# Kernel optimization log

Hardware: AMD Instinct MI355X
Metric: run time of the kernel (lower is better)

## Reference

```python
import jax, jax.numpy as jnp
from jax import lax
import numpy as np

CIN, COUT, K, STYLE_DIM = 256, 256, 3, 512
N_LAYERS = 4
TYPES = ("same", "upsample", "same", "downsample")
SCALE = 1.0 / float(np.sqrt(CIN * K ** 2))  # source uses kernel_size**2 even in 1D
EPS = 1e-8
_BK = np.array([1.0, 3.0, 3.0, 1.0], dtype=np.float32)
BLUR_K = _BK / _BK.sum()  # normalized FIR kernel, len 4


def _blur(x, kern, pad):
    # x: (B, C, L); depthwise FIR correlation after zero-padding (upfirdn1d, up=down=1)
    B, C, _ = x.shape
    xp = jnp.pad(x, ((0, 0), (0, 0), (pad[0], pad[1])))
    w = jnp.broadcast_to(kern.astype(x.dtype)[None, None, :], (C, 1, kern.shape[0]))
    return lax.conv_general_dilated(xp, w, (1,), 'VALID', feature_group_count=C,
                                    dimension_numbers=('NCH', 'OIH', 'NCH'))


def _conv_same(x, w):
    # x: (Cin, L), w: (Cout, Cin, K); padding = (K-1)//2, stride 1
    p = (K - 1) // 2
    return lax.conv_general_dilated(x[None], w, (1,), [(p, p)],
                                    dimension_numbers=('NCH', 'OIH', 'NCH'))[0]


def _conv_down(x, w):
    # stride-2 valid conv (padding handled by preceding blur)
    return lax.conv_general_dilated(x[None], w, (2,), 'VALID',
                                    dimension_numbers=('NCH', 'OIH', 'NCH'))[0]


def _conv_up(x, w_t):
    # torch conv_transpose1d(stride=2, padding=0); w_t: (Cin, Cout, K)
    return lax.conv_transpose(x[None], w_t, (2,), 'VALID',
                              dimension_numbers=('NCH', 'IOH', 'NCH'),
                              transpose_kernel=True)[0]


def _layer(x, style, w, b, mw, mb, typ):
    # style modulation: s = Linear(style) -> (B, Cin)
    s = style @ mw.T + mb
    weight = (SCALE * w) * s[:, None, :, None]              # (B, Cout, Cin, K)
    demod = lax.rsqrt(jnp.sum(weight * weight, axis=(2, 3)) + EPS)
    weight = weight * demod[:, :, None, None]
    blur_k = jnp.asarray(BLUR_K)
    if typ == 'same':
        out = jax.vmap(_conv_same)(x, weight) + b[None, :, None]
    elif typ == 'upsample':
        # bias added by conv_transpose BEFORE blur (kernel_scale=2, pad=(1,1) for k=3, kb=4)
        out = jax.vmap(_conv_up)(x, weight.transpose(0, 2, 1, 3)) + b[None, :, None]
        out = _blur(out, 2.0 * blur_k, (1, 1))
    elif typ == 'downsample':
        # blur first (kernel_scale=1, pad=(2,2) for k=3, kb=4), then stride-2 conv
        xb = _blur(x, blur_k, (2, 2))
        out = jax.vmap(_conv_down)(xb, weight) + b[None, :, None]
    else:
        raise NotImplementedError(typ)
    return out


def setup_inputs() -> dict:
    key = jax.random.key(0)
    ks = jax.random.split(key, 6)
    B, L = 16, 4096
    return {
        'x': jax.random.normal(ks[0], (B, CIN, L), dtype=jnp.float32),
        'style': jax.random.normal(ks[1], (B, STYLE_DIM), dtype=jnp.float32),
        'weights': jax.random.normal(ks[2], (N_LAYERS, COUT, CIN, K), dtype=jnp.float32),
        'biases': jax.random.normal(ks[3], (N_LAYERS, COUT), dtype=jnp.float32) * 0.1,
        'mod_w': jax.random.normal(ks[4], (N_LAYERS, CIN, STYLE_DIM), dtype=jnp.float32) / np.sqrt(STYLE_DIM),
        'mod_b': 1.0 + 0.1 * jax.random.normal(ks[5], (N_LAYERS, CIN), dtype=jnp.float32),
    }


def reference(x, style, weights, biases, mod_w, mod_b):
    out = x
    for i, typ in enumerate(TYPES):
        out = _layer(out, style, weights[i], biases[i], mod_w[i], mod_b[i], typ)
    return out
```

## Files before the change

kernel.cpp:

```cpp
#include <hip/hip_runtime.h>
#include <math.h>
#include <stddef.h>

#define CIN 256
#define COUT 256
#define SD 512
#define NB 16
#define KSCALE (1.0f / 48.0f)
#define MEPS 1e-8f
#define SRROW 8320

typedef __attribute__((ext_vector_type(8))) short short8;
typedef __attribute__((ext_vector_type(4))) float floatx4;
typedef unsigned short ushort;

__device__ inline ushort f2bf(float f) {
    union { float f; unsigned int u; } v; v.f = f;
    unsigned int u = v.u;
    return (ushort)((u + 0x7FFFu + ((u >> 16) & 1u)) >> 16);
}
__device__ inline float bf2f(ushort h) {
    union { unsigned int u; float f; } v; v.u = ((unsigned int)h) << 16;
    return v.f;
}

__device__ inline void gload16(const ushort* g, ushort* l) {
    __builtin_amdgcn_global_load_lds(
        (const __attribute__((address_space(1))) unsigned int*)g,
        (__attribute__((address_space(3))) unsigned int*)l,
        16, 0, 0);
}

__global__ __launch_bounds__(256) void mod_k(
    const float* __restrict__ style, const float* __restrict__ weights,
    const float* __restrict__ mod_w, const float* __restrict__ mod_b,
    float* __restrict__ s_all, float* __restrict__ demod_all)
{
    int layer = blockIdx.x >> 4;
    int b = blockIdx.x & 15;
    int t = threadIdx.x;
    __shared__ float st[SD];
    __shared__ float s2[CIN];

    for (int j = t; j < SD; j += 256) st[j] = style[b * SD + j];
    __syncthreads();

    const float* mw = mod_w + ((size_t)layer * CIN + t) * SD;
    float acc = 0.f;
    for (int j = 0; j < SD; ++j) acc += mw[j] * st[j];
    float s = acc + mod_b[layer * CIN + t];
    s_all[((size_t)layer * NB + b) * CIN + t] = s;
    s2[t] = s * s;
    __syncthreads();

    const float* wr = weights + ((size_t)layer * COUT + t) * (CIN * 3);
    float d = 0.f;
    for (int ci = 0; ci < CIN; ++ci) {
        float w0 = wr[ci * 3 + 0], w1 = wr[ci * 3 + 1], w2 = wr[ci * 3 + 2];
        d += (w0 * w0 + w1 * w1 + w2 * w2) * s2[ci];
    }
    demod_all[((size_t)layer * NB + b) * CIN + t] = rsqrtf(KSCALE * KSCALE * d + MEPS);
}

__global__ __launch_bounds__(256) void wprep_k(
    const float* __restrict__ weights, ushort* __restrict__ Wbf)
{
    int layer = blockIdx.y;
    int idx = blockIdx.x * 256 + threadIdx.x;
    int a = idx >> 8, c = idx & 255;
    ushort* wl = Wbf + (size_t)layer * 196608;
    if (layer == 1) {
        const float* src = weights + ((size_t)1 * 196608) + ((size_t)c * 256 + a) * 3;
        #pragma unroll
        for (int k = 0; k < 3; ++k)
            wl[(size_t)k * 65536 + a * 256 + c] = f2bf(src[k]);
    } else {
        const float* src = weights + ((size_t)layer * 196608) + ((size_t)a * 256 + c) * 3;
        #pragma unroll
        for (int k = 0; k < 3; ++k)
            wl[(size_t)a * 768 + k * 256 + c] = f2bf(src[k]);
    }
}

__global__ __launch_bounds__(256) void xprep_k(
    const float* __restrict__ x, const float* __restrict__ s0,
    ushort* __restrict__ Tout)
{
    __shared__ ushort lt[64 * 72];
    int l0 = blockIdx.x * 64, ci0 = blockIdx.y * 64;
    int b = blockIdx.z;
    int t = threadIdx.x;
    const float* xb = x + (size_t)b * CIN * 4096;
    const float* sb = s0 + b * CIN;

    for (int idx = t; idx < 64 * 64; idx += 256) {
        int ci = idx >> 6, lc = idx & 63;
        float v = xb[(size_t)(ci0 + ci) * 4096 + l0 + lc] * sb[ci0 + ci];
        lt[lc * 72 + ci] = f2bf(v);
    }
    __syncthreads();
    ushort* ob = Tout + (size_t)b * SRROW * 256;
    for (int idx = t; idx < 64 * 8; idx += 256) {
        int lc = idx >> 3, ch = idx & 7;
        short8 v = *(const short8*)&lt[lc * 72 + ch * 8];
        *(short8*)&ob[(size_t)(l0 + lc) * 256 + ci0 + ch * 8] = v;
    }
}

__global__ __launch_bounds__(256) void guard_k(
    ushort* __restrict__ T, int rowA, int rowB)
{
    int b = blockIdx.x;
    ushort* base = T + (size_t)b * SRROW * 256;
    base[(size_t)rowA * 256 + threadIdx.x] = 0;
    base[(size_t)rowB * 256 + threadIdx.x] = 0;
}

__global__ __launch_bounds__(256) void blur_bf16_k(
    const ushort* __restrict__ in, int Lin,
    ushort* __restrict__ outp, int Lout,
    const float* __restrict__ scale,
    int pad, float c0, float c1, float c2, float c3)
{
    int b = blockIdx.y;
    int idx = blockIdx.x * 256 + threadIdx.x;
    if (idx >= Lout * 32) return;
    int row = idx >> 5, ci = (idx & 31) * 8;
    const ushort* ib = in + (size_t)b * SRROW * 256;
    float acc[8] = {};
    int base = row - pad;
    float cf[4] = {c0, c1, c2, c3};
    #pragma unroll
    for (int i = 0; i < 4; ++i) {
        int r = base + i;
        if (r >= 0 && r < Lin) {
            short8 v = *(const short8*)&ib[(size_t)r * 256 + ci];
            #pragma unroll
            for (int j = 0; j < 8; ++j) acc[j] += cf[i] * bf2f((ushort)v[j]);
        }
    }
    short8 o;
    #pragma unroll
    for (int j = 0; j < 8; ++j) {
        float sv = scale[b * CIN + ci + j];
        o[j] = (short)f2bf(acc[j] * sv);
    }
    *(short8*)&outp[((size_t)b * SRROW + row) * 256 + ci] = o;
}

__global__ __launch_bounds__(512, 4) void conv_same_mfma(
    const ushort* __restrict__ Tin,
    const ushort* __restrict__ Wl,
    const float* __restrict__ dm, const float* __restrict__ post,
    const float* __restrict__ bias,
    ushort* __restrict__ Tout)
{
    __shared__ __align__(16) ushort S[29184];
    ushort* Xs = S;
    ushort* Ws = S + 16896;
    int l0 = blockIdx.x * 256;
    int cot = blockIdx.y * 64;
    int b = blockIdx.z;
    int t = threadIdx.x;
    int lane = t & 63, wv = t >> 6;
    int lr = lane & 15, lg = lane >> 4;
    int lrow = lane >> 3, cg = lane & 7;

    const ushort* Tb = Tin + (size_t)b * SRROW * 256;

    floatx4 acc[4][2];
    #pragma unroll
    for (int i = 0; i < 4; ++i) { acc[i][0] = (floatx4)0.f; acc[i][1] = (floatx4)0.f; }

    for (int ci0 = 0; ci0 < 256; ci0 += 64) {
        __syncthreads();
        for (int i = wv; i < 24; i += 8) {
            int wr = i * 8 + lrow;
            int co = wr & 63, tap = wr >> 6;
            gload16(Wl + (size_t)(cot + co) * 768 + tap * 256 + ci0 + ((cg ^ (co & 7)) * 8),
                    Ws + i * 512);
        }
        for (int i = wv; i < 33; i += 8) {
            int row = i * 8 + lrow;
            gload16(Tb + (ptrdiff_t)(l0 - 1 + row) * 256 + ci0 + ((cg ^ (row & 7)) * 8),
                    Xs + i * 512);
        }
        __syncthreads();
        #pragma unroll
        for (int tap = 0; tap < 3; ++tap)
            #pragma unroll
            for (int kk = 0; kk < 2; ++kk) {
                short8 a[4];
                #pragma unroll
                for (int mf = 0; mf < 4; ++mf)
                    a[mf] = *(const short8*)&Ws[(tap * 64 + mf * 16 + lr) * 64 + ((kk * 32 + lg * 8) ^ ((lr & 7) * 8))];
                short8 bf[2];
                #pragma unroll
                for (int nf = 0; nf < 2; ++nf) {
                    int row = wv * 32 + nf * 16 + lr + tap;
                    bf[nf] = *(const short8*)&Xs[row * 64 + ((kk * 32 + lg * 8) ^ ((row & 7) * 8))];
                }
                #pragma unroll
                for (int mf = 0; mf < 4; ++mf)
                    #pragma unroll
                    for (int nf = 0; nf < 2; ++nf)
                        acc[mf][nf] = __builtin_amdgcn_mfma_f32_16x16x32_bf16(a[mf], bf[nf], acc[mf][nf], 0, 0, 0);
            }
    }

    __syncthreads();
    ushort* Ot = S;
    #pragma unroll
    for (int mf = 0; mf < 4; ++mf)
        #pragma unroll
        for (int nf = 0; nf < 2; ++nf)
            #pragma unroll
            for (int rg = 0; rg < 4; ++rg) {
                int lo = wv * 32 + nf * 16 + lr;
                int co = mf * 16 + lg * 4 + rg;
                float dmv = dm[b * COUT + cot + co] * KSCALE;
                float v = acc[mf][nf][rg] * dmv + bias[cot + co];
                if (post) v *= post[b * COUT + cot + co] * KSCALE;
                Ot[lo * 72 + co] = f2bf(v);
            }
    __syncthreads();
    ushort* ob = Tout + (size_t)b * SRROW * 256;
    for (int idx = t; idx < 256 * 8; idx += 512) {
        int lo = idx >> 3, ch = idx & 7;
        short8 v = *(const short8*)&Ot[lo * 72 + ch * 8];
        *(short8*)&ob[(size_t)(l0 + lo) * 256 + cot + ch * 8] = v;
    }
}

__global__ __launch_bounds__(512, 4) void upconv_mfma(
    const ushort* __restrict__ Tin, int Lout,
    const ushort* __restrict__ Wl,
    const float* __restrict__ s, const float* __restrict__ bias,
    ushort* __restrict__ Tout)
{
    __shared__ __align__(16) ushort S[29184];
    ushort* Xs = S;
    ushort* Ws = S + 16896;
    int m0 = blockIdx.x * 256;
    int ot = blockIdx.y * 64;
    int b = blockIdx.z;
    int t = threadIdx.x;
    int lane = t & 63, wv = t >> 6;
    int lr = lane & 15, lg = lane >> 4;
    int lrow = lane >> 3, cg = lane & 7;

    const ushort* Tb = Tin + (size_t)b * SRROW * 256;

    floatx4 aE[4][2], aO[4][2];
    #pragma unroll
    for (int i = 0; i < 4; ++i)
        #pragma unroll
        for (int j = 0; j < 2; ++j) { aE[i][j] = (floatx4)0.f; aO[i][j] = (floatx4)0.f; }

    for (int ci0 = 0; ci0 < 256; ci0 += 64) {
        __syncthreads();
        for (int i = wv; i < 24; i += 8) {
            int wr = i * 8 + lrow;
            int o = wr & 63, tap = wr >> 6;
            gload16(Wl + (size_t)tap * 65536 + (size_t)(ot + o) * 256 + ci0 + ((cg ^ (o & 7)) * 8),
                    Ws + i * 512);
        }
        for (int i = wv; i < 33; i += 8) {
            int row = i * 8 + lrow;
            gload16(Tb + (ptrdiff_t)(m0 - 1 + row) * 256 + ci0 + ((cg ^ (row & 7)) * 8),
                    Xs + i * 512);
        }
        __syncthreads();
        #pragma unroll
        for (int kk = 0; kk < 2; ++kk) {
            short8 bm1[2], bm[2];
            #pragma unroll
            for (int nf = 0; nf < 2; ++nf) {
                int r0 = wv * 32 + nf * 16 + lr;
                int ci = kk * 32 + lg * 8;
                bm1[nf] = *(const short8*)&Xs[r0 * 64 + (ci ^ ((r0 & 7) * 8))];
                int r1 = r0 + 1;
                bm[nf]  = *(const short8*)&Xs[r1 * 64 + (ci ^ ((r1 & 7) * 8))];
            }
            #pragma unroll
            for (int tap = 0; tap < 3; ++tap) {
                short8 a[4];
                #pragma unroll
                for (int mf = 0; mf < 4; ++mf)
                    a[mf] = *(const short8*)&Ws[(tap * 64 + mf * 16 + lr) * 64 + ((kk * 32 + lg * 8) ^ ((lr & 7) * 8))];
                #pragma unroll
                for (int mf = 0; mf < 4; ++mf)
                    #pragma unroll
                    for (int nf = 0; nf < 2; ++nf) {
                        if (tap == 0) aE[mf][nf] = __builtin_amdgcn_mfma_f32_16x16x32_bf16(a[mf], bm[nf],  aE[mf][nf], 0, 0, 0);
                        if (tap == 2) aE[mf][nf] = __builtin_amdgcn_mfma_f32_16x16x32_bf16(a[mf], bm1[nf], aE[mf][nf], 0, 0, 0);
                        if (tap == 1) aO[mf][nf] = __builtin_amdgcn_mfma_f32_16x16x32_bf16(a[mf], bm[nf],  aO[mf][nf], 0, 0, 0);
                    }
            }
        }
    }

    ushort* Ot = S;
    ushort* ob = Tout + (size_t)b * SRROW * 256;
    __syncthreads();
    if (wv < 4) {
        #pragma unroll
        for (int mf = 0; mf < 4; ++mf)
            #pragma unroll
            for (int nf = 0; nf < 2; ++nf)
                #pragma unroll
                for (int rg = 0; rg < 4; ++rg) {
                    int mloc = wv * 32 + nf * 16 + lr;
                    int co = mf * 16 + lg * 4 + rg;
                    float sv = s[b * COUT + ot + co];
                    float bi = bias[ot + co];
                    Ot[(2 * mloc) * 72 + co]     = f2bf(aE[mf][nf][rg] * sv + bi);
                    Ot[(2 * mloc + 1) * 72 + co] = f2bf(aO[mf][nf][rg] * sv + bi);
                }
    }
    __syncthreads();
    for (int idx = t; idx < 256 * 8; idx += 512) {
        int lo = idx >> 3, ch = idx & 7;
        int n = 2 * m0 + lo;
        if (n < Lout) {
            short8 v = *(const short8*)&Ot[lo * 72 + ch * 8];
            *(short8*)&ob[(size_t)n * 256 + ot + ch * 8] = v;
        }
    }
    __syncthreads();
    if (wv >= 4) {
        #pragma unroll
        for (int mf = 0; mf < 4; ++mf)
            #pragma unroll
            for (int nf = 0; nf < 2; ++nf)
                #pragma unroll
                for (int rg = 0; rg < 4; ++rg) {
                    int mloc = wv * 32 + nf * 16 + lr;
                    int co = mf * 16 + lg * 4 + rg;
                    float sv = s[b * COUT + ot + co];
                    float bi = bias[ot + co];
                    Ot[(2 * mloc - 256) * 72 + co] = f2bf(aE[mf][nf][rg] * sv + bi);
                    Ot[(2 * mloc - 255) * 72 + co] = f2bf(aO[mf][nf][rg] * sv + bi);
                }
    }
    __syncthreads();
    for (int idx = t; idx < 256 * 8; idx += 512) {
        int lo = idx >> 3, ch = idx & 7;
        int n = 2 * m0 + 256 + lo;
        if (n < Lout) {
            short8 v = *(const short8*)&Ot[lo * 72 + ch * 8];
            *(short8*)&ob[(size_t)n * 256 + ot + ch * 8] = v;
        }
    }
}

__global__ __launch_bounds__(512, 4) void conv_down_mfma(
    const ushort* __restrict__ Tin,
    const ushort* __restrict__ Wl,
    const float* __restrict__ dm, const float* __restrict__ bias,
    float* __restrict__ outp)
{
    __shared__ __align__(16) ushort S[29184];
    ushort* Xs = S;
    ushort* Ws = S + 16896;
    int l0 = blockIdx.x * 128;
    int cot = blockIdx.y * 64;
    int b = blockIdx.z;
    int t = threadIdx.x;
    int lane = t & 63, wv = t >> 6;
    int lr = lane & 15, lg = lane >> 4;
    int lrow = lane >> 3, cg = lane & 7;

    const ushort* Tb = Tin + (size_t)b * SRROW * 256;

    floatx4 acc[4];
    #pragma unroll
    for (int i = 0; i < 4; ++i) acc[i] = (floatx4)0.f;

    for (int ci0 = 0; ci0 < 256; ci0 += 64) {
        __syncthreads();
        for (int i = wv; i < 24; i += 8) {
            int wr = i * 8 + lrow;
            int co = wr & 63, tap = wr >> 6;
            gload16(Wl + (size_t)(cot + co) * 768 + tap * 256 + ci0 + ((cg ^ (co & 7)) * 8),
                    Ws + i * 512);
        }
        for (int i = wv; i < 33; i += 8) {
            int row = i * 8 + lrow;
            gload16(Tb + (ptrdiff_t)(2 * l0 + row) * 256 + ci0 + ((cg ^ (row & 7)) * 8),
                    Xs + i * 512);
        }
        __syncthreads();
        #pragma unroll
        for (int tap = 0; tap < 3; ++tap)
            #pragma unroll
            for (int kk = 0; kk < 2; ++kk) {
                short8 a[4];
                #pragma unroll
                for (int mf = 0; mf < 4; ++mf)
                    a[mf] = *(const short8*)&Ws[(tap * 64 + mf * 16 + lr) * 64 + ((kk * 32 + lg * 8) ^ ((lr & 7) * 8))];
                int row = 2 * (wv * 16 + lr) + tap;
                short8 bf = *(const short8*)&Xs[row * 64 + ((kk * 32 + lg * 8) ^ ((row & 7) * 8))];
                #pragma unroll
                for (int mf = 0; mf < 4; ++mf)
                    acc[mf] = __builtin_amdgcn_mfma_f32_16x16x32_bf16(a[mf], bf, acc[mf], 0, 0, 0);
            }
    }

    float* ob = outp + (size_t)b * COUT * 4096;
    #pragma unroll
    for (int mf = 0; mf < 4; ++mf)
        #pragma unroll
        for (int rg = 0; rg < 4; ++rg) {
            int co = cot + mf * 16 + lg * 4 + rg;
            int l = l0 + wv * 16 + lr;
            float dmv = dm[b * COUT + co] * KSCALE;
            ob[(size_t)co * 4096 + l] = acc[mf][rg] * dmv + bias[co];
        }
}

extern "C" void kernel_launch(void* const* d_in, const int* in_sizes, int n_in,
                              void* d_out, int out_size, void* d_ws, size_t ws_size,
                              hipStream_t stream) {
    const float* x       = (const float*)d_in[0];
    const float* style   = (const float*)d_in[1];
    const float* weights = (const float*)d_in[2];
    const float* biases  = (const float*)d_in[3];
    const float* mod_w   = (const float*)d_in[4];
    const float* mod_b   = (const float*)d_in[5];
    float* out = (float*)d_out;

    float* s_all = (float*)d_ws;
    float* demod_all = s_all + 4 * NB * CIN;
    const size_t WBF_OFF = 131072;
    const size_t BUF_OFF = WBF_OFF + 1572864;
    ushort* Wbf = (ushort*)((char*)d_ws + WBF_OFF);
    ushort* bufBase = (ushort*)((char*)d_ws + BUF_OFF);

    const int SL = NB * CIN;
    const size_t perSampleB = (size_t)2 * SRROW * 256 * sizeof(ushort);
    size_t availB = ws_size > BUF_OFF ? ws_size - BUF_OFF : 0;
    int g = (int)(availB / perSampleB);
    if (g < 1) g = 1;
    if (g > NB) g = NB;

    const size_t sElems = (size_t)SRROW * 256;
    ushort* bufAU = bufBase;
    ushort* bufBU = bufBase + (size_t)g * sElems;
    ushort* bufA = bufAU + 256;
    ushort* bufB = bufBU + 256;

    mod_k<<<64, 256, 0, stream>>>(style, weights, mod_w, mod_b, s_all, demod_all);
    wprep_k<<<dim3(256, 4), 256, 0, stream>>>(weights, Wbf);

    for (int b0 = 0; b0 < NB; b0 += g) {
        int gb = NB - b0 < g ? NB - b0 : g;

        xprep_k<<<dim3(64, 4, gb), 256, 0, stream>>>(
            x + (size_t)b0 * CIN * 4096, s_all + 0 * SL + b0 * CIN, bufA);
        guard_k<<<gb, 256, 0, stream>>>(bufAU, 0, 4097);

        conv_same_mfma<<<dim3(16, 4, gb), 512, 0, stream>>>(
            bufA, Wbf + 0 * 196608,
            demod_all + 0 * SL + b0 * CIN, demod_all + 1 * SL + b0 * CIN,
            biases + 0 * COUT, bufB);
        guard_k<<<gb, 256, 0, stream>>>(bufBU, 0, 4097);

        upconv_mfma<<<dim3(17, 4, gb), 512, 0, stream>>>(
            bufB, 8193, Wbf + 1 * 196608,
            s_all + 1 * SL + b0 * CIN, biases + 1 * COUT, bufA);

        blur_bf16_k<<<dim3(1024, gb), 256, 0, stream>>>(
            bufA, 8193, bufB, 8192, s_all + 2 * SL + b0 * CIN,
            1, 0.25f, 0.75f, 0.75f, 0.25f);
        guard_k<<<gb, 256, 0, stream>>>(bufBU, 0, 8193);

        conv_same_mfma<<<dim3(32, 4, gb), 512, 0, stream>>>(
            bufB, Wbf + 2 * 196608,
            demod_all + 2 * SL + b0 * CIN, (const float*)nullptr,
            biases + 2 * COUT, bufA);

        blur_bf16_k<<<dim3(1025, gb), 256, 0, stream>>>(
            bufA, 8192, bufB, 8193, s_all + 3 * SL + b0 * CIN,
            2, 0.125f, 0.375f, 0.375f, 0.125f);

        conv_down_mfma<<<dim3(32, 4, gb), 512, 0, stream>>>(
            bufB, Wbf + 3 * 196608,
            demod_all + 3 * SL + b0 * CIN, biases + 3 * COUT,
            out + (size_t)b0 * COUT * 4096);
    }
}
```

Measured before the change: 302.0 us.

## Double-buffer LDS staging with 32-channel chunks in all three MFMA conv kernels

Replaces the single-buffer, 64-channel-per-iteration LDS staging with a two-buffer ping-pong over 32-channel chunks. The next chunk's global-to-LDS loads are issued before the MFMAs on the current chunk, so memory latency can overlap compute, and there is one barrier per chunk instead of two. The swizzle is narrowed to 4 slots to fit 64-byte rows. This doubles the number of chunk iterations and slightly enlarges shared memory, which could affect occupancy and raise LDS bank conflicts under the narrower swizzle.

Result: slower. 336.3 us (+11.4%).

```diff
diff --git a/kernel.cpp b/kernel.cpp
--- a/kernel.cpp
+++ b/kernel.cpp
@@ -155,16 +155,14 @@
     const float* __restrict__ bias,
     ushort* __restrict__ Tout)
 {
-    __shared__ __align__(16) ushort S[29184];
-    ushort* Xs = S;
-    ushort* Ws = S + 16896;
+    __shared__ __align__(16) ushort S[29696];
     int l0 = blockIdx.x * 256;
     int cot = blockIdx.y * 64;
     int b = blockIdx.z;
     int t = threadIdx.x;
     int lane = t & 63, wv = t >> 6;
     int lr = lane & 15, lg = lane >> 4;
-    int lrow = lane >> 3, cg = lane & 7;
+    int srow = lane >> 2, sslot = lane & 3;
 
     const ushort* Tb = Tin + (size_t)b * SRROW * 256;
 
@@ -172,43 +170,52 @@
     #pragma unroll
     for (int i = 0; i < 4; ++i) { acc[i][0] = (floatx4)0.f; acc[i][1] = (floatx4)0.f; }
 
-    for (int ci0 = 0; ci0 < 256; ci0 += 64) {
+    auto STAGE = [&](int ci0, int buf) {
+        ushort* Xd = S + buf * 8704;
+        ushort* Wd = S + 17408 + buf * 6144;
+        for (int i = wv; i < 29; i += 8) {
+            if (i < 17) {
+                int row = i * 16 + srow;
+                gload16(Tb + (ptrdiff_t)(l0 - 1 + row) * 256 + ci0 + ((sslot ^ (row & 3)) * 8),
+                        Xd + i * 512);
+            } else {
+                int wr = (i - 17) * 16 + srow;
+                int co = wr & 63, tap = wr >> 6;
+                gload16(Wl + (size_t)(cot + co) * 768 + tap * 256 + ci0 + ((sslot ^ (wr & 3)) * 8),
+                        Wd + (i - 17) * 512);
+            }
+        }
+    };
+
+    STAGE(0, 0);
+    __syncthreads();
+    for (int c = 0; c < 8; ++c) {
+        ushort* Xc = S + (c & 1) * 8704;
+        ushort* Wc = S + 17408 + (c & 1) * 6144;
+        if (c < 7) STAGE((c + 1) * 32, (c + 1) & 1);
+        #pragma unroll
+        for (int tap = 0; tap < 3; ++tap) {
+            short8 a[4];
+            #pragma unroll
+            for (int mf = 0; mf < 4; ++mf) {
+                int wr = tap * 64 + mf * 16 + lr;
+                a[mf] = *(const short8*)&Wc[wr * 32 + ((lg * 8) ^ ((wr & 3) * 8))];
+            }
+            short8 bf[2];
+            #pragma unroll
+            for (int nf = 0; nf < 2; ++nf) {
+                int row = wv * 32 + nf * 16 + lr + tap;
+                bf[nf] = *(const short8*)&Xc[row * 32 + ((lg * 8) ^ ((row & 3) * 8))];
+            }
+            #pragma unroll
+            for (int mf = 0; mf < 4; ++mf)
+                #pragma unroll
+                for (int nf = 0; nf < 2; ++nf)
+                    acc[mf][nf] = __builtin_amdgcn_mfma_f32_16x16x32_bf16(a[mf], bf[nf], acc[mf][nf], 0, 0, 0);
+        }
         __syncthreads();
-        for (int i = wv; i < 24; i += 8) {
-            int wr = i * 8 + lrow;
-            int co = wr & 63, tap = wr >> 6;
-            gload16(Wl + (size_t)(cot + co) * 768 + tap * 256 + ci0 + ((cg ^ (co & 7)) * 8),
-                    Ws + i * 512);
-        }
-        for (int i = wv; i < 33; i += 8) {
-            int row = i * 8 + lrow;
-            gload16(Tb + (ptrdiff_t)(l0 - 1 + row) * 256 + ci0 + ((cg ^ (row & 7)) * 8),
-                    Xs + i * 512);
-        }
-        __syncthreads();
-        #pragma unroll
-        for (int tap = 0; tap < 3; ++tap)
-            #pragma unroll
-            for (int kk = 0; kk < 2; ++kk) {
-                short8 a[4];
-                #pragma unroll
-                for (int mf = 0; mf < 4; ++mf)
-                    a[mf] = *(const short8*)&Ws[(tap * 64 + mf * 16 + lr) * 64 + ((kk * 32 + lg * 8) ^ ((lr & 7) * 8))];
-                short8 bf[2];
-                #pragma unroll
-                for (int nf = 0; nf < 2; ++nf) {
-                    int row = wv * 32 + nf * 16 + lr + tap;
-                    bf[nf] = *(const short8*)&Xs[row * 64 + ((kk * 32 + lg * 8) ^ ((row & 7) * 8))];
-                }
-                #pragma unroll
-                for (int mf = 0; mf < 4; ++mf)
-                    #pragma unroll
-                    for (int nf = 0; nf < 2; ++nf)
-                        acc[mf][nf] = __builtin_amdgcn_mfma_f32_16x16x32_bf16(a[mf], bf[nf], acc[mf][nf], 0, 0, 0);
-            }
-    }
-
-    __syncthreads();
+    }
+
     ushort* Ot = S;
     #pragma unroll
     for (int mf = 0; mf < 4; ++mf)
@@ -238,16 +245,14 @@
     const float* __restrict__ s, const float* __restrict__ bias,
     ushort* __restrict__ Tout)
 {
-    __shared__ __align__(16) ushort S[29184];
-    ushort* Xs = S;
-    ushort* Ws = S + 16896;
+    __shared__ __align__(16) ushort S[29696];
     int m0 = blockIdx.x * 256;
     int ot = blockIdx.y * 64;
     int b = blockIdx.z;
     int t = threadIdx.x;
     int lane = t & 63, wv = t >> 6;
     int lr = lane & 15, lg = lane >> 4;
-    int lrow = lane >> 3, cg = lane & 7;
+    int srow = lane >> 2, sslot = lane & 3;
 
     const ushort* Tb = Tin + (size_t)b * SRROW * 256;
 
@@ -257,52 +262,59 @@
         #pragma unroll
         for (int j = 0; j < 2; ++j) { aE[i][j] = (floatx4)0.f; aO[i][j] = (floatx4)0.f; }
 
-    for (int ci0 = 0; ci0 < 256; ci0 += 64) {
+    auto STAGE = [&](int ci0, int buf) {
+        ushort* Xd = S + buf * 8704;
+        ushort* Wd = S + 17408 + buf * 6144;
+        for (int i = wv; i < 29; i += 8) {
+            if (i < 17) {
+                int row = i * 16 + srow;
+                gload16(Tb + (ptrdiff_t)(m0 - 1 + row) * 256 + ci0 + ((sslot ^ (row & 3)) * 8),
+                        Xd + i * 512);
+            } else {
+                int wr = (i - 17) * 16 + srow;
+                int o = wr & 63, tap = wr >> 6;
+                gload16(Wl + (size_t)tap * 65536 + (size_t)(ot + o) * 256 + ci0 + ((sslot ^ (wr & 3)) * 8),
+                        Wd + (i - 17) * 512);
+            }
+        }
+    };
+
+    STAGE(0, 0);
+    __syncthreads();
+    for (int c = 0; c < 8; ++c) {
+        ushort* Xc = S + (c & 1) * 8704;
+        ushort* Wc = S + 17408 + (c & 1) * 6144;
+        if (c < 7) STAGE((c + 1) * 32, (c + 1) & 1);
+        short8 bm1[2], bm[2];
+        #pragma unroll
+        for (int nf = 0; nf < 2; ++nf) {
+            int r0 = wv * 32 + nf * 16 + lr;
+            bm1[nf] = *(const short8*)&Xc[r0 * 32 + ((lg * 8) ^ ((r0 & 3) * 8))];
+            int r1 = r0 + 1;
+            bm[nf]  = *(const short8*)&Xc[r1 * 32 + ((lg * 8) ^ ((r1 & 3) * 8))];
+        }
+        #pragma unroll
+        for (int tap = 0; tap < 3; ++tap) {
+            short8 a[4];
+            #pragma unroll
+            for (int mf = 0; mf < 4; ++mf) {
+                int wr = tap * 64 + mf * 16 + lr;
+                a[mf] = *(const short8*)&Wc[wr * 32 + ((lg * 8) ^ ((wr & 3) * 8))];
+            }
+            #pragma unroll
+            for (int mf = 0; mf < 4; ++mf)
+                #pragma unroll
+                for (int nf = 0; nf < 2; ++nf) {
+                    if (tap == 0) aE[mf][nf] = __builtin_amdgcn_mfma_f32_16x16x32_bf16(a[mf], bm[nf],  aE[mf][nf], 0, 0, 0);
+                    if (tap == 2) aE[mf][nf] = __builtin_amdgcn_mfma_f32_16x16x32_bf16(a[mf], bm1[nf], aE[mf][nf], 0, 0, 0);
+                    if (tap == 1) aO[mf][nf] = __builtin_amdgcn_mfma_f32_16x16x32_bf16(a[mf], bm[nf],  aO[mf][nf], 0, 0, 0);
+                }
+        }
         __syncthreads();
-        for (int i = wv; i < 24; i += 8) {
-            int wr = i * 8 + lrow;
-            int o = wr & 63, tap = wr >> 6;
-            gload16(Wl + (size_t)tap * 65536 + (size_t)(ot + o) * 256 + ci0 + ((cg ^ (o & 7)) * 8),
-                    Ws + i * 512);
-        }
-        for (int i = wv; i < 33; i += 8) {
-            int row = i * 8 + lrow;
-            gload16(Tb + (ptrdiff_t)(m0 - 1 + row) * 256 + ci0 + ((cg ^ (row & 7)) * 8),
-                    Xs + i * 512);
-        }
-        __syncthreads();
-        #pragma unroll
-        for (int kk = 0; kk < 2; ++kk) {
-            short8 bm1[2], bm[2];
-            #pragma unroll
-            for (int nf = 0; nf < 2; ++nf) {
-                int r0 = wv * 32 + nf * 16 + lr;
-                int ci = kk * 32 + lg * 8;
-                bm1[nf] = *(const short8*)&Xs[r0 * 64 + (ci ^ ((r0 & 7) * 8))];
-                int r1 = r0 + 1;
-                bm[nf]  = *(const short8*)&Xs[r1 * 64 + (ci ^ ((r1 & 7) * 8))];
-            }
-            #pragma unroll
-            for (int tap = 0; tap < 3; ++tap) {
-                short8 a[4];
-                #pragma unroll
-                for (int mf = 0; mf < 4; ++mf)
-                    a[mf] = *(const short8*)&Ws[(tap * 64 + mf * 16 + lr) * 64 + ((kk * 32 + lg * 8) ^ ((lr & 7) * 8))];
-                #pragma unroll
-                for (int mf = 0; mf < 4; ++mf)
-                    #pragma unroll
-                    for (int nf = 0; nf < 2; ++nf) {
-                        if (tap == 0) aE[mf][nf] = __builtin_amdgcn_mfma_f32_16x16x32_bf16(a[mf], bm[nf],  aE[mf][nf], 0, 0, 0);
-                        if (tap == 2) aE[mf][nf] = __builtin_amdgcn_mfma_f32_16x16x32_bf16(a[mf], bm1[nf], aE[mf][nf], 0, 0, 0);
-                        if (tap == 1) aO[mf][nf] = __builtin_amdgcn_mfma_f32_16x16x32_bf16(a[mf], bm[nf],  aO[mf][nf], 0, 0, 0);
-                    }
-            }
-        }
     }
 
     ushort* Ot = S;
     ushort* ob = Tout + (size_t)b * SRROW * 256;
-    __syncthreads();
     if (wv < 4) {
         #pragma unroll
         for (int mf = 0; mf < 4; ++mf)
@@ -360,16 +372,14 @@
     const float* __restrict__ dm, const float* __restrict__ bias,
     float* __restrict__ outp)
 {
-    __shared__ __align__(16) ushort S[29184];
-    ushort* Xs = S;
-    ushort* Ws = S + 16896;
+    __shared__ __align__(16) ushort S[29696];
     int l0 = blockIdx.x * 128;
     int cot = blockIdx.y * 64;
     int b = blockIdx.z;
     int t = threadIdx.x;
     int lane = t & 63, wv = t >> 6;
     int lr = lane & 15, lg = lane >> 4;
-    int lrow = lane >> 3, cg = lane & 7;
+    int srow = lane >> 2, sslot = lane & 3;
 
     const ushort* Tb = Tin + (size_t)b * SRROW * 256;
 
@@ -377,34 +387,44 @@
     #pragma unroll
     for (int i = 0; i < 4; ++i) acc[i] = (floatx4)0.f;
 
-    for (int ci0 = 0; ci0 < 256; ci0 += 64) {
+    auto STAGE = [&](int ci0, int buf) {
+        ushort* Xd = S + buf * 8704;
+        ushort* Wd = S + 17408 + buf * 6144;
+        for (int i = wv; i < 29; i += 8) {
+            if (i < 17) {
+                int row = i * 16 + srow;
+                gload16(Tb + (ptrdiff_t)(2 * l0 + row) * 256 + ci0 + ((sslot ^ (row & 3)) * 8),
+                        Xd + i * 512);
+            } else {
+                int wr = (i - 17) * 16 + srow;
+                int co = wr & 63, tap = wr >> 6;
+                gload16(Wl + (size_t)(cot + co) * 768 + tap * 256 + ci0 + ((sslot ^ (wr & 3)) * 8),
+                        Wd + (i - 17) * 512);
+            }
+        }
+    };
+
+    STAGE(0, 0);
+    __syncthreads();
+    for (int c = 0; c < 8; ++c) {
+        ushort* Xc = S + (c & 1) * 8704;
+        ushort* Wc = S + 17408 + (c & 1) * 6144;
+        if (c < 7) STAGE((c + 1) * 32, (c + 1) & 1);
+        #pragma unroll
+        for (int tap = 0; tap < 3; ++tap) {
+            short8 a[4];
+            #pragma unroll
+            for (int mf = 0; mf < 4; ++mf) {
+                int wr = tap * 64 + mf * 16 + lr;
+                a[mf] = *(const short8*)&Wc[wr * 32 + ((lg * 8) ^ ((wr & 3) * 8))];
+            }
+            int row = 2 * (wv * 16 + lr) + tap;
+            short8 bf = *(const short8*)&Xc[row * 32 + ((lg * 8) ^ ((row & 3) * 8))];
+            #pragma unroll
+            for (int mf = 0; mf < 4; ++mf)
+                acc[mf] = __builtin_amdgcn_mfma_f32_16x16x32_bf16(a[mf], bf, acc[mf], 0, 0, 0);
+        }
         __syncthreads();
-        for (int i = wv; i < 24; i += 8) {
-            int wr = i * 8 + lrow;
-            int co = wr & 63, tap = wr >> 6;
-            gload16(Wl + (size_t)(cot + co) * 768 + tap * 256 + ci0 + ((cg ^ (co & 7)) * 8),
-                    Ws + i * 512);
-        }
-        for (int i = wv; i < 33; i += 8) {
-            int row = i * 8 + lrow;
-            gload16(Tb + (ptrdiff_t)(2 * l0 + row) * 256 + ci0 + ((cg ^ (row & 7)) * 8),
-                    Xs + i * 512);
-        }
-        __syncthreads();
-        #pragma unroll
-        for (int tap = 0; tap < 3; ++tap)
-            #pragma unroll
-            for (int kk = 0; kk < 2; ++kk) {
-                short8 a[4];
-                #pragma unroll
-                for (int mf = 0; mf < 4; ++mf)
-                    a[mf] = *(const short8*)&Ws[(tap * 64 + mf * 16 + lr) * 64 + ((kk * 32 + lg * 8) ^ ((lr & 7) * 8))];
-                int row = 2 * (wv * 16 + lr) + tap;
-                short8 bf = *(const short8*)&Xs[row * 64 + ((kk * 32 + lg * 8) ^ ((row & 7) * 8))];
-                #pragma unroll
-                for (int mf = 0; mf < 4; ++mf)
-                    acc[mf] = __builtin_amdgcn_mfma_f32_16x16x32_bf16(a[mf], bf, acc[mf], 0, 0, 0);
-            }
     }
 
     float* ob = outp + (size_t)b * COUT * 4096;
```

## Double L-tile per block in conv kernels with 32-wide channel chunks and deinterleaved stride-2 layout

Applied to the files above, without the earlier changes.

conv_same_mfma now computes 512 output positions per block (4x4 MFMA fragments per wave) and conv_down_mfma 256 positions, so each weight tile loaded into LDS is reused across twice as many positions. The input-channel chunk shrinks from 64 to 32, which changes the swizzle and reduces LDS use. The epilogue is written out in two halves through the same LDS staging buffer. For the stride-2 conv, even and odd input rows are stored in separate LDS regions so each tap reads contiguous rows. The trade-offs are more accumulator registers per thread, half as many blocks in the grid, and twice as many K-loop iterations and barriers.

After: 315.5 us. +4.5%, slower.

```diff
diff --git a/kernel.cpp b/kernel.cpp
--- a/kernel.cpp
+++ b/kernel.cpp
@@ -155,80 +155,107 @@
     const float* __restrict__ bias,
     ushort* __restrict__ Tout)
 {
-    __shared__ __align__(16) ushort S[29184];
+    __shared__ __align__(16) ushort S[23040];
     ushort* Xs = S;
     ushort* Ws = S + 16896;
-    int l0 = blockIdx.x * 256;
+    int l0 = blockIdx.x * 512;
     int cot = blockIdx.y * 64;
     int b = blockIdx.z;
     int t = threadIdx.x;
     int lane = t & 63, wv = t >> 6;
     int lr = lane & 15, lg = lane >> 4;
-    int lrow = lane >> 3, cg = lane & 7;
+    int srow = lane >> 2, sslot = lane & 3;
 
     const ushort* Tb = Tin + (size_t)b * SRROW * 256;
 
-    floatx4 acc[4][2];
+    floatx4 acc[4][4];
     #pragma unroll
-    for (int i = 0; i < 4; ++i) { acc[i][0] = (floatx4)0.f; acc[i][1] = (floatx4)0.f; }
-
-    for (int ci0 = 0; ci0 < 256; ci0 += 64) {
+    for (int i = 0; i < 4; ++i)
+        #pragma unroll
+        for (int j = 0; j < 4; ++j) acc[i][j] = (floatx4)0.f;
+
+    for (int ci0 = 0; ci0 < 256; ci0 += 32) {
         __syncthreads();
-        for (int i = wv; i < 24; i += 8) {
-            int wr = i * 8 + lrow;
-            int co = wr & 63, tap = wr >> 6;
-            gload16(Wl + (size_t)(cot + co) * 768 + tap * 256 + ci0 + ((cg ^ (co & 7)) * 8),
-                    Ws + i * 512);
-        }
-        for (int i = wv; i < 33; i += 8) {
-            int row = i * 8 + lrow;
-            gload16(Tb + (ptrdiff_t)(l0 - 1 + row) * 256 + ci0 + ((cg ^ (row & 7)) * 8),
-                    Xs + i * 512);
+        for (int i = wv; i < 45; i += 8) {
+            if (i < 33) {
+                int row = i * 16 + srow;
+                gload16(Tb + (ptrdiff_t)(l0 - 1 + row) * 256 + ci0 + ((sslot ^ ((row >> 1) & 3)) * 8),
+                        Xs + i * 512);
+            } else {
+                int wr = (i - 33) * 16 + srow;
+                int co = wr & 63, tap = wr >> 6;
+                gload16(Wl + (size_t)(cot + co) * 768 + tap * 256 + ci0 + ((sslot ^ ((wr >> 1) & 3)) * 8),
+                        Ws + (i - 33) * 512);
+            }
         }
         __syncthreads();
         #pragma unroll
-        for (int tap = 0; tap < 3; ++tap)
-            #pragma unroll
-            for (int kk = 0; kk < 2; ++kk) {
-                short8 a[4];
-                #pragma unroll
-                for (int mf = 0; mf < 4; ++mf)
-                    a[mf] = *(const short8*)&Ws[(tap * 64 + mf * 16 + lr) * 64 + ((kk * 32 + lg * 8) ^ ((lr & 7) * 8))];
-                short8 bf[2];
-                #pragma unroll
-                for (int nf = 0; nf < 2; ++nf) {
-                    int row = wv * 32 + nf * 16 + lr + tap;
-                    bf[nf] = *(const short8*)&Xs[row * 64 + ((kk * 32 + lg * 8) ^ ((row & 7) * 8))];
+        for (int tap = 0; tap < 3; ++tap) {
+            short8 a[4];
+            #pragma unroll
+            for (int mf = 0; mf < 4; ++mf) {
+                int wr = tap * 64 + mf * 16 + lr;
+                a[mf] = *(const short8*)&Ws[wr * 32 + ((lg ^ ((wr >> 1) & 3)) * 8)];
+            }
+            short8 bf[4];
+            #pragma unroll
+            for (int nf = 0; nf < 4; ++nf) {
+                int row = wv * 64 + nf * 16 + lr + tap;
+                bf[nf] = *(const short8*)&Xs[row * 32 + ((lg ^ ((row >> 1) & 3)) * 8)];
+            }
+            #pragma unroll
+            for (int mf = 0; mf < 4; ++mf)
+                #pragma unroll
+                for (int nf = 0; nf < 4; ++nf)
+                    acc[mf][nf] = __builtin_amdgcn_mfma_f32_16x16x32_bf16(a[mf], bf[nf], acc[mf][nf], 0, 0, 0);
+        }
+    }
+
+    ushort* Ot = S;
+    __syncthreads();
+    if (wv < 4) {
+        #pragma unroll
+        for (int mf = 0; mf < 4; ++mf)
+            #pragma unroll
+            for (int nf = 0; nf < 4; ++nf)
+                #pragma unroll
+                for (int rg = 0; rg < 4; ++rg) {
+                    int lo = wv * 64 + nf * 16 + lr;
+                    int co = mf * 16 + lg * 4 + rg;
+                    float dmv = dm[b * COUT + cot + co] * KSCALE;
+                    float v = acc[mf][nf][rg] * dmv + bias[cot + co];
+                    if (post) v *= post[b * COUT + cot + co] * KSCALE;
+                    Ot[lo * 72 + co] = f2bf(v);
                 }
-                #pragma unroll
-                for (int mf = 0; mf < 4; ++mf)
-                    #pragma unroll
-                    for (int nf = 0; nf < 2; ++nf)
-                        acc[mf][nf] = __builtin_amdgcn_mfma_f32_16x16x32_bf16(a[mf], bf[nf], acc[mf][nf], 0, 0, 0);
-            }
-    }
-
-    __syncthreads();
-    ushort* Ot = S;
-    #pragma unroll
-    for (int mf = 0; mf < 4; ++mf)
-        #pragma unroll
-        for (int nf = 0; nf < 2; ++nf)
-            #pragma unroll
-            for (int rg = 0; rg < 4; ++rg) {
-                int lo = wv * 32 + nf * 16 + lr;
-                int co = mf * 16 + lg * 4 + rg;
-                float dmv = dm[b * COUT + cot + co] * KSCALE;
-                float v = acc[mf][nf][rg] * dmv + bias[cot + co];
-                if (post) v *= post[b * COUT + cot + co] * KSCALE;
-                Ot[lo * 72 + co] = f2bf(v);
-            }
+    }
     __syncthreads();
     ushort* ob = Tout + (size_t)b * SRROW * 256;
     for (int idx = t; idx < 256 * 8; idx += 512) {
         int lo = idx >> 3, ch = idx & 7;
         short8 v = *(const short8*)&Ot[lo * 72 + ch * 8];
         *(short8*)&ob[(size_t)(l0 + lo) * 256 + cot + ch * 8] = v;
+    }
+    __syncthreads();
+    if (wv >= 4) {
+        #pragma unroll
+        for (int mf = 0; mf < 4; ++mf)
+            #pragma unroll
+            for (int nf = 0; nf < 4; ++nf)
+                #pragma unroll
+                for (int rg = 0; rg < 4; ++rg) {
+                    int lo = wv * 64 + nf * 16 + lr - 256;
+                    int co = mf * 16 + lg * 4 + rg;
+                    float dmv = dm[b * COUT + cot + co] * KSCALE;
+                    float v = acc[mf][nf][rg] * dmv + bias[cot + co];
+                    if (post) v *= post[b * COUT + cot + co] * KSCALE;
+                    Ot[lo * 72 + co] = f2bf(v);
+                }
+    }
+    __syncthreads();
+    for (int idx = t; idx < 256 * 8; idx += 512) {
+        int lo = idx >> 3, ch = idx & 7;
+        short8 v = *(const short8*)&Ot[lo * 72 + ch * 8];
+        *(short8*)&ob[(size_t)(l0 + 256 + lo) * 256 + cot + ch * 8] = v;
     }
 }
 
@@ -360,63 +387,74 @@
     const float* __restrict__ dm, const float* __restrict__ bias,
     float* __restrict__ outp)
 {
-    __shared__ __align__(16) ushort S[29184];
+    __shared__ __align__(16) ushort S[23040];
     ushort* Xs = S;
     ushort* Ws = S + 16896;
-    int l0 = blockIdx.x * 128;
+    int l0 = blockIdx.x * 256;
     int cot = blockIdx.y * 64;
     int b = blockIdx.z;
     int t = threadIdx.x;
     int lane = t & 63, wv = t >> 6;
     int lr = lane & 15, lg = lane >> 4;
-    int lrow = lane >> 3, cg = lane & 7;
+    int srow = lane >> 2, sslot = lane & 3;
 
     const ushort* Tb = Tin + (size_t)b * SRROW * 256;
 
-    floatx4 acc[4];
+    floatx4 acc[4][2];
     #pragma unroll
-    for (int i = 0; i < 4; ++i) acc[i] = (floatx4)0.f;
-
-    for (int ci0 = 0; ci0 < 256; ci0 += 64) {
+    for (int i = 0; i < 4; ++i) { acc[i][0] = (floatx4)0.f; acc[i][1] = (floatx4)0.f; }
+
+    for (int ci0 = 0; ci0 < 256; ci0 += 32) {
         __syncthreads();
-        for (int i = wv; i < 24; i += 8) {
-            int wr = i * 8 + lrow;
-            int co = wr & 63, tap = wr >> 6;
-            gload16(Wl + (size_t)(cot + co) * 768 + tap * 256 + ci0 + ((cg ^ (co & 7)) * 8),
-                    Ws + i * 512);
-        }
-        for (int i = wv; i < 33; i += 8) {
-            int row = i * 8 + lrow;
-            gload16(Tb + (ptrdiff_t)(2 * l0 + row) * 256 + ci0 + ((cg ^ (row & 7)) * 8),
-                    Xs + i * 512);
+        for (int i = wv; i < 45; i += 8) {
+            if (i < 33) {
+                int ldr = i * 16 + srow;
+                int grow = (ldr < 264) ? (2 * ldr) : (2 * (ldr - 264) + 1);
+                gload16(Tb + (ptrdiff_t)(2 * l0 + grow) * 256 + ci0 + ((sslot ^ ((ldr >> 1) & 3)) * 8),
+                        Xs + i * 512);
+            } else {
+                int wr = (i - 33) * 16 + srow;
+                int co = wr & 63, tap = wr >> 6;
+                gload16(Wl + (size_t)(cot + co) * 768 + tap * 256 + ci0 + ((sslot ^ ((wr >> 1) & 3)) * 8),
+                        Ws + (i - 33) * 512);
+            }
         }
         __syncthreads();
         #pragma unroll
-        for (int tap = 0; tap < 3; ++tap)
-            #pragma unroll
-            for (int kk = 0; kk < 2; ++kk) {
-                short8 a[4];
-                #pragma unroll
-                for (int mf = 0; mf < 4; ++mf)
-                    a[mf] = *(const short8*)&Ws[(tap * 64 + mf * 16 + lr) * 64 + ((kk * 32 + lg * 8) ^ ((lr & 7) * 8))];
-                int row = 2 * (wv * 16 + lr) + tap;
-                short8 bf = *(const short8*)&Xs[row * 64 + ((kk * 32 + lg * 8) ^ ((row & 7) * 8))];
-                #pragma unroll
-                for (int mf = 0; mf < 4; ++mf)
-                    acc[mf] = __builtin_amdgcn_mfma_f32_16x16x32_bf16(a[mf], bf, acc[mf], 0, 0, 0);
-            }
+        for (int tap = 0; tap < 3; ++tap) {
+            short8 a[4];
+            #pragma unroll
+            for (int mf = 0; mf < 4; ++mf) {
+                int wr = tap * 64 + mf * 16 + lr;
+                a[mf] = *(const short8*)&Ws[wr * 32 + ((lg ^ ((wr >> 1) & 3)) * 8)];
+            }
+            short8 bf[2];
+            #pragma unroll
+            for (int nf = 0; nf < 2; ++nf) {
+                int l = wv * 32 + nf * 16 + lr;
+                int ldr = (tap == 1) ? (264 + l) : (l + (tap >> 1));
+                bf[nf] = *(const short8*)&Xs[ldr * 32 + ((lg ^ ((ldr >> 1) & 3)) * 8)];
+            }
+            #pragma unroll
+            for (int mf = 0; mf < 4; ++mf)
+                #pragma unroll
+                for (int nf = 0; nf < 2; ++nf)
+                    acc[mf][nf] = __builtin_amdgcn_mfma_f32_16x16x32_bf16(a[mf], bf[nf], acc[mf][nf], 0, 0, 0);
+        }
     }
 
     float* ob = outp + (size_t)b * COUT * 4096;
     #pragma unroll
     for (int mf = 0; mf < 4; ++mf)
         #pragma unroll
-        for (int rg = 0; rg < 4; ++rg) {
-            int co = cot + mf * 16 + lg * 4 + rg;
-            int l = l0 + wv * 16 + lr;
-            float dmv = dm[b * COUT + co] * KSCALE;
-            ob[(size_t)co * 4096 + l] = acc[mf][rg] * dmv + bias[co];
-        }
+        for (int nf = 0; nf < 2; ++nf)
+            #pragma unroll
+            for (int rg = 0; rg < 4; ++rg) {
+                int co = cot + mf * 16 + lg * 4 + rg;
+                int l = l0 + wv * 32 + nf * 16 + lr;
+                float dmv = dm[b * COUT + co] * KSCALE;
+                ob[(size_t)co * 4096 + l] = acc[mf][nf][rg] * dmv + bias[co];
+            }
 }
 
 extern "C" void kernel_launch(void* const* d_in, const int* in_sizes, int n_in,
@@ -460,7 +498,7 @@
             x + (size_t)b0 * CIN * 4096, s_all + 0 * SL + b0 * CIN, bufA);
         guard_k<<<gb, 256, 0, stream>>>(bufAU, 0, 4097);
 
-        conv_same_mfma<<<dim3(16, 4, gb), 512, 0, stream>>>(
+        conv_same_mfma<<<dim3(8, 4, gb), 512, 0, stream>>>(
             bufA, Wbf + 0 * 196608,
             demod_all + 0 * SL + b0 * CIN, demod_all + 1 * SL + b0 * CIN,
             biases + 0 * COUT, bufB);
@@ -475,7 +513,7 @@
             1, 0.25f, 0.75f, 0.75f, 0.25f);
         guard_k<<<gb, 256, 0, stream>>>(bufBU, 0, 8193);
 
-        conv_same_mfma<<<dim3(32, 4, gb), 512, 0, stream>>>(
+        conv_same_mfma<<<dim3(16, 4, gb), 512, 0, stream>>>(
             bufB, Wbf + 2 * 196608,
             demod_all + 2 * SL + b0 * CIN, (const float*)nullptr,
             biases + 2 * COUT, bufA);
@@ -484,7 +522,7 @@
             bufA, 8192, bufB, 8193, s_all + 3 * SL + b0 * CIN,
             2, 0.125f, 0.375f, 0.375f, 0.125f);
 
-        conv_down_mfma<<<dim3(32, 4, gb), 512, 0, stream>>>(
+        conv_down_mfma<<<dim3(16, 4, gb), 512, 0, stream>>>(
             bufB, Wbf + 3 * 196608,
             demod_all + 3 * SL + b0 * CIN, biases + 3 * COUT,
             out + (size_t)b0 * COUT * 4096);
```

## Fold downsample blur into stride-2 conv weights as a 6-tap kernel

Applied to the files above, without the earlier changes.

The change removes the separate blur pass before the downsample conv. It convolves the 3-tap weights with the 4-tap blur filter during weight prep, giving a 6-tap stride-2 conv that reads the un-blurred layer-2 output directly. The style scaling for layer 3 now happens in the epilogue of the previous conv. Guard rows are widened to two zero rows on each side, and the down kernel uses 32-channel K chunks with smaller LDS so more blocks can be resident. This cuts one full-tensor bf16 read/write pass and a launch, but the down conv now does twice the MFMA work per output.

New measurement: 313.2 us. 3.7% more time.

```diff
diff --git a/kernel.cpp b/kernel.cpp
--- a/kernel.cpp
+++ b/kernel.cpp
@@ -68,14 +68,30 @@
     int layer = blockIdx.y;
     int idx = blockIdx.x * 256 + threadIdx.x;
     int a = idx >> 8, c = idx & 255;
-    ushort* wl = Wbf + (size_t)layer * 196608;
     if (layer == 1) {
-        const float* src = weights + ((size_t)1 * 196608) + ((size_t)c * 256 + a) * 3;
+        ushort* wl = Wbf + 196608;
+        const float* src = weights + 196608 + ((size_t)c * 256 + a) * 3;
         #pragma unroll
         for (int k = 0; k < 3; ++k)
             wl[(size_t)k * 65536 + a * 256 + c] = f2bf(src[k]);
+    } else if (layer == 3) {
+        ushort* wl = Wbf + 589824;
+        const float* src = weights + (size_t)3 * 196608 + ((size_t)a * 256 + c) * 3;
+        float w0 = src[0], w1 = src[1], w2 = src[2];
+        const float c2k[4] = {0.125f, 0.375f, 0.375f, 0.125f};
+        float w6[6];
+        w6[0] = w0 * c2k[0];
+        w6[1] = w0 * c2k[1] + w1 * c2k[0];
+        w6[2] = w0 * c2k[2] + w1 * c2k[1] + w2 * c2k[0];
+        w6[3] = w0 * c2k[3] + w1 * c2k[2] + w2 * c2k[1];
+        w6[4] = w1 * c2k[3] + w2 * c2k[2];
+        w6[5] = w2 * c2k[3];
+        #pragma unroll
+        for (int j = 0; j < 6; ++j)
+            wl[(size_t)a * 1536 + j * 256 + c] = f2bf(w6[j]);
     } else {
-        const float* src = weights + ((size_t)layer * 196608) + ((size_t)a * 256 + c) * 3;
+        ushort* wl = Wbf + (layer == 0 ? 0 : 393216);
+        const float* src = weights + (size_t)layer * 196608 + ((size_t)a * 256 + c) * 3;
         #pragma unroll
         for (int k = 0; k < 3; ++k)
             wl[(size_t)a * 768 + k * 256 + c] = f2bf(src[k]);
@@ -108,12 +124,14 @@
 }
 
 __global__ __launch_bounds__(256) void guard_k(
-    ushort* __restrict__ T, int rowA, int rowB)
+    ushort* __restrict__ T, int r0, int r1, int r2, int r3)
 {
     int b = blockIdx.x;
     ushort* base = T + (size_t)b * SRROW * 256;
-    base[(size_t)rowA * 256 + threadIdx.x] = 0;
-    base[(size_t)rowB * 256 + threadIdx.x] = 0;
+    base[(size_t)r0 * 256 + threadIdx.x] = 0;
+    base[(size_t)r1 * 256 + threadIdx.x] = 0;
+    base[(size_t)r2 * 256 + threadIdx.x] = 0;
+    base[(size_t)r3 * 256 + threadIdx.x] = 0;
 }
 
 __global__ __launch_bounds__(256) void blur_bf16_k(
@@ -149,9 +167,9 @@
 }
 
 __global__ __launch_bounds__(512, 4) void conv_same_mfma(
-    const ushort* __restrict__ Tin,
+    const ushort* __restrict__ Tin, int Lmax,
     const ushort* __restrict__ Wl,
-    const float* __restrict__ dm, const float* __restrict__ post,
+    const float* __restrict__ dm, const float* __restrict__ post, float postScale,
     const float* __restrict__ bias,
     ushort* __restrict__ Tout)
 {
@@ -182,7 +200,9 @@
         }
         for (int i = wv; i < 33; i += 8) {
             int row = i * 8 + lrow;
-            gload16(Tb + (ptrdiff_t)(l0 - 1 + row) * 256 + ci0 + ((cg ^ (row & 7)) * 8),
+            int dr = l0 - 1 + row;
+            if (dr > Lmax) dr = Lmax;
+            gload16(Tb + (ptrdiff_t)dr * 256 + ci0 + ((cg ^ (row & 7)) * 8),
                     Xs + i * 512);
         }
         __syncthreads();
@@ -220,7 +240,7 @@
                 int co = mf * 16 + lg * 4 + rg;
                 float dmv = dm[b * COUT + cot + co] * KSCALE;
                 float v = acc[mf][nf][rg] * dmv + bias[cot + co];
-                if (post) v *= post[b * COUT + cot + co] * KSCALE;
+                if (post) v *= post[b * COUT + cot + co] * postScale;
                 Ot[lo * 72 + co] = f2bf(v);
             }
     __syncthreads();
@@ -354,22 +374,22 @@
     }
 }
 
-__global__ __launch_bounds__(512, 4) void conv_down_mfma(
+__global__ __launch_bounds__(512, 6) void conv_down_mfma(
     const ushort* __restrict__ Tin,
     const ushort* __restrict__ Wl,
     const float* __restrict__ dm, const float* __restrict__ bias,
     float* __restrict__ outp)
 {
-    __shared__ __align__(16) ushort S[29184];
+    __shared__ __align__(16) ushort S[20992];
     ushort* Xs = S;
-    ushort* Ws = S + 16896;
+    ushort* Ws = S + 8704;
     int l0 = blockIdx.x * 128;
     int cot = blockIdx.y * 64;
     int b = blockIdx.z;
     int t = threadIdx.x;
     int lane = t & 63, wv = t >> 6;
     int lr = lane & 15, lg = lane >> 4;
-    int lrow = lane >> 3, cg = lane & 7;
+    int srow = lane >> 2, sslot = lane & 3;
 
     const ushort* Tb = Tin + (size_t)b * SRROW * 256;
 
@@ -377,34 +397,37 @@
     #pragma unroll
     for (int i = 0; i < 4; ++i) acc[i] = (floatx4)0.f;
 
-    for (int ci0 = 0; ci0 < 256; ci0 += 64) {
+    for (int ci0 = 0; ci0 < 256; ci0 += 32) {
         __syncthreads();
-        for (int i = wv; i < 24; i += 8) {
-            int wr = i * 8 + lrow;
-            int co = wr & 63, tap = wr >> 6;
-            gload16(Wl + (size_t)(cot + co) * 768 + tap * 256 + ci0 + ((cg ^ (co & 7)) * 8),
-                    Ws + i * 512);
-        }
-        for (int i = wv; i < 33; i += 8) {
-            int row = i * 8 + lrow;
-            gload16(Tb + (ptrdiff_t)(2 * l0 + row) * 256 + ci0 + ((cg ^ (row & 7)) * 8),
-                    Xs + i * 512);
+        for (int i = wv; i < 41; i += 8) {
+            if (i < 17) {
+                int ldr = i * 16 + srow;
+                int dr = 2 * l0 - 2 + ldr;
+                if (dr > 8193) dr = 8193;
+                gload16(Tb + (ptrdiff_t)dr * 256 + ci0 + ((sslot ^ ((ldr >> 1) & 3)) * 8),
+                        Xs + i * 512);
+            } else {
+                int wr = (i - 17) * 16 + srow;
+                int co = wr & 63, tp = wr >> 6;
+                gload16(Wl + (size_t)(cot + co) * 1536 + tp * 256 + ci0 + ((sslot ^ ((wr >> 1) & 3)) * 8),
+                        Ws + (i - 17) * 512);
+            }
         }
         __syncthreads();
         #pragma unroll
-        for (int tap = 0; tap < 3; ++tap)
-            #pragma unroll
-            for (int kk = 0; kk < 2; ++kk) {
-                short8 a[4];
-                #pragma unroll
-                for (int mf = 0; mf < 4; ++mf)
-                    a[mf] = *(const short8*)&Ws[(tap * 64 + mf * 16 + lr) * 64 + ((kk * 32 + lg * 8) ^ ((lr & 7) * 8))];
-                int row = 2 * (wv * 16 + lr) + tap;
-                short8 bf = *(const short8*)&Xs[row * 64 + ((kk * 32 + lg * 8) ^ ((row & 7) * 8))];
-                #pragma unroll
-                for (int mf = 0; mf < 4; ++mf)
-                    acc[mf] = __builtin_amdgcn_mfma_f32_16x16x32_bf16(a[mf], bf, acc[mf], 0, 0, 0);
+        for (int tp = 0; tp < 6; ++tp) {
+            short8 a[4];
+            #pragma unroll
+            for (int mf = 0; mf < 4; ++mf) {
+                int wr = tp * 64 + mf * 16 + lr;
+                a[mf] = *(const short8*)&Ws[wr * 32 + ((lg ^ ((wr >> 1) & 3)) * 8)];
             }
+            int row = 2 * (wv * 16 + lr) + tp;
+            short8 bf = *(const short8*)&Xs[row * 32 + ((lg ^ ((row >> 1) & 3)) * 8)];
+            #pragma unroll
+            for (int mf = 0; mf < 4; ++mf)
+                acc[mf] = __builtin_amdgcn_mfma_f32_16x16x32_bf16(a[mf], bf, acc[mf], 0, 0, 0);
+        }
     }
 
     float* ob = outp + (size_t)b * COUT * 4096;
@@ -433,7 +456,7 @@
     float* s_all = (float*)d_ws;
     float* demod_all = s_all + 4 * NB * CIN;
     const size_t WBF_OFF = 131072;
-    const size_t BUF_OFF = WBF_OFF + 1572864;
+    const size_t BUF_OFF = WBF_OFF + 1966080;
     ushort* Wbf = (ushort*)((char*)d_ws + WBF_OFF);
     ushort* bufBase = (ushort*)((char*)d_ws + BUF_OFF);
 
@@ -447,8 +470,8 @@
     const size_t sElems = (size_t)SRROW * 256;
     ushort* bufAU = bufBase;
     ushort* bufBU = bufBase + (size_t)g * sElems;
-    ushort* bufA = bufAU + 256;
-    ushort* bufB = bufBU + 256;
+    ushort* bufA = bufAU + 512;
+    ushort* bufB = bufBU + 512;
 
     mod_k<<<64, 256, 0, stream>>>(style, weights, mod_w, mod_b, s_all, demod_all);
     wprep_k<<<dim3(256, 4), 256, 0, stream>>>(weights, Wbf);
@@ -458,34 +481,31 @@
 
         xprep_k<<<dim3(64, 4, gb), 256, 0, stream>>>(
             x + (size_t)b0 * CIN * 4096, s_all + 0 * SL + b0 * CIN, bufA);
-        guard_k<<<gb, 256, 0, stream>>>(bufAU, 0, 4097);
+        guard_k<<<gb, 256, 0, stream>>>(bufAU, 0, 1, 4098, 4099);
 
         conv_same_mfma<<<dim3(16, 4, gb), 512, 0, stream>>>(
-            bufA, Wbf + 0 * 196608,
-            demod_all + 0 * SL + b0 * CIN, demod_all + 1 * SL + b0 * CIN,
+            bufA, 4097, Wbf + 0,
+            demod_all + 0 * SL + b0 * CIN, demod_all + 1 * SL + b0 * CIN, KSCALE,
             biases + 0 * COUT, bufB);
-        guard_k<<<gb, 256, 0, stream>>>(bufBU, 0, 4097);
+        guard_k<<<gb, 256, 0, stream>>>(bufBU, 0, 1, 4098, 4099);
 
         upconv_mfma<<<dim3(17, 4, gb), 512, 0, stream>>>(
-            bufB, 8193, Wbf + 1 * 196608,
+            bufB, 8193, Wbf + 196608,
             s_all + 1 * SL + b0 * CIN, biases + 1 * COUT, bufA);
 
         blur_bf16_k<<<dim3(1024, gb), 256, 0, stream>>>(
             bufA, 8193, bufB, 8192, s_all + 2 * SL + b0 * CIN,
             1, 0.25f, 0.75f, 0.75f, 0.25f);
-        guard_k<<<gb, 256, 0, stream>>>(bufBU, 0, 8193);
+        guard_k<<<gb, 256, 0, stream>>>(bufBU, 0, 1, 8194, 8195);
 
         conv_same_mfma<<<dim3(32, 4, gb), 512, 0, stream>>>(
-            bufB, Wbf + 2 * 196608,
-            demod_all + 2 * SL + b0 * CIN, (const float*)nullptr,
+            bufB, 8193, Wbf + 393216,
+            demod_all + 2 * SL + b0 * CIN, s_all + 3 * SL + b0 * CIN, 1.0f,
             biases + 2 * COUT, bufA);
-
-        blur_bf16_k<<<dim3(1025, gb), 256, 0, stream>>>(
-            bufA, 8192, bufB, 8193, s_all + 3 * SL + b0 * CIN,
-            2, 0.125f, 0.375f, 0.375f, 0.125f);
+        guard_k<<<gb, 256, 0, stream>>>(bufAU, 0, 1, 8194, 8195);
 
         conv_down_mfma<<<dim3(32, 4, gb), 512, 0, stream>>>(
-            bufB, Wbf + 3 * 196608,
+            bufA, Wbf + 589824,
             demod_all + 3 * SL + b0 * CIN, biases + 3 * COUT,
             out + (size_t)b0 * COUT * 4096);
     }
```
